# Performance work log

Measured on AMD Instinct MI355X. Metric: run time of the kernel, lower is better.

## Reference

```python
import jax, jax.numpy as jnp
import numpy as np

EMBED_DIM = 1024
NUM_HEADS = 16
HEAD_DIM = EMBED_DIM // NUM_HEADS


def setup_inputs() -> dict:
    key = jax.random.key(0)
    ks = jax.random.split(key, 9)
    B, T, D = 4, 2048, EMBED_DIM
    s = 1.0 / np.sqrt(D)
    inp = {
        "x": jax.random.normal(ks[0], (B, T, D), dtype=jnp.float32),
        "Wq": jax.random.normal(ks[1], (D, D), dtype=jnp.float32) * s,
        "bq": jnp.zeros((D,), dtype=jnp.float32),
        "Wk": jax.random.normal(ks[2], (D, D), dtype=jnp.float32) * s,
        "bk": jnp.zeros((D,), dtype=jnp.float32),
        "Wv": jax.random.normal(ks[3], (D, D), dtype=jnp.float32) * s,
        "bv": jnp.zeros((D,), dtype=jnp.float32),
        "Wo": jax.random.normal(ks[4], (D, D), dtype=jnp.float32) * s,
        "bo": jnp.zeros((D,), dtype=jnp.float32),
    }
    return inp


def _attn(x, Wq, bq, Wk, bk, Wv, bv, Wo, bo):
    B, T, D = x.shape
    H, Hd = NUM_HEADS, HEAD_DIM
    # projections: Linear uses y = x @ W^T + b; here W stored as (D, D) acting as W^T already
    q = (x @ Wq + bq).reshape(B, T, H, Hd).transpose(0, 2, 1, 3)  # [B,H,T,Hd]
    k = (x @ Wk + bk).reshape(B, T, H, Hd).transpose(0, 2, 1, 3)
    v = (x @ Wv + bv).reshape(B, T, H, Hd).transpose(0, 2, 1, 3)
    scores = jnp.einsum("bhqd,bhkd->bhqk", q, k) / np.sqrt(Hd)  # [B,H,T,T]
    causal = jnp.tril(jnp.ones((T, T), dtype=bool))
    scores = jnp.where(causal, scores, -jnp.inf)
    w = jax.nn.softmax(scores, axis=-1)
    out = jnp.einsum("bhqk,bhkd->bhqd", w, v)  # [B,H,T,Hd]
    out = out.transpose(0, 2, 1, 3).reshape(B, T, D)
    return out @ Wo + bo


def reference(x, Wq, bq, Wk, bk, Wv, bv, Wo, bo):
    return _attn(x, Wq, bq, Wk, bk, Wv, bv, Wo, bo)
```

## Files before the change

kernel.cpp:

```cpp
#include <hip/hip_runtime.h>
#include <cstdint>
#include <cstddef>

#define DI __device__ __forceinline__

typedef unsigned short u16;
typedef short bf16x8 __attribute__((ext_vector_type(8)));
typedef unsigned short u16x8 __attribute__((ext_vector_type(8)));
typedef float f32x4 __attribute__((ext_vector_type(4)));

static constexpr int DMODEL = 1024, T = 2048, BB = 4, NH = 16, HD = 64;
static constexpr int M = BB * T;

static constexpr size_t XB_OFF = 0;
static constexpr size_t WT_OFF = (size_t)M * DMODEL;
static constexpr size_t Q_OFF  = WT_OFF + 4ull * DMODEL * DMODEL;
static constexpr size_t K_OFF  = Q_OFF + (size_t)M * DMODEL;
static constexpr size_t V_OFF  = K_OFF + (size_t)M * DMODEL;
static constexpr size_t O_OFF  = XB_OFF;

DI u16 f2bf(float x) {
  unsigned int u = __builtin_bit_cast(unsigned int, x);
  u += 0x7fffu + ((u >> 16) & 1u);
  return (u16)(u >> 16);
}

DI unsigned int cvtpk_bf16(float a, float b) {
  unsigned int r;
  asm("v_cvt_pk_bf16_f32 %0, %1, %2" : "=v"(r) : "v"(a), "v"(b));
  return r;
}

DI void gld_lds16(const void* g, void* l) {
  __builtin_amdgcn_global_load_lds(
      (const __attribute__((address_space(1))) void*)g,
      (__attribute__((address_space(3))) void*)l, 16, 0, 0);
}

__global__ void k_cast(const float* __restrict__ in, u16* __restrict__ out) {
  size_t i = (size_t)(blockIdx.x * 256 + threadIdx.x) * 8;
  float4 a = *(const float4*)(in + i);
  float4 b = *(const float4*)(in + i + 4);
  u16x8 v;
  v[0] = f2bf(a.x); v[1] = f2bf(a.y); v[2] = f2bf(a.z); v[3] = f2bf(a.w);
  v[4] = f2bf(b.x); v[5] = f2bf(b.y); v[6] = f2bf(b.z); v[7] = f2bf(b.w);
  *(u16x8*)(out + i) = v;
}

__global__ void k_transw(const float* __restrict__ Wq, const float* __restrict__ Wk,
                         const float* __restrict__ Wv, const float* __restrict__ Wo,
                         u16* __restrict__ WtBase) {
  __shared__ u16 tile[32][33];
  const int z = blockIdx.z;
  const float* W = z == 0 ? Wq : (z == 1 ? Wk : (z == 2 ? Wv : Wo));
  u16* Wt = WtBase + (size_t)z * DMODEL * DMODEL;
  int tx = threadIdx.x, ty = threadIdx.y;
  int c = blockIdx.x * 32 + tx;
#pragma unroll
  for (int i = 0; i < 4; ++i) {
    int r = blockIdx.y * 32 + ty + i * 8;
    tile[ty + i * 8][tx] = f2bf(W[(size_t)r * DMODEL + c]);
  }
  __syncthreads();
#pragma unroll
  for (int i = 0; i < 4; ++i) {
    int rw = blockIdx.x * 32 + ty + i * 8;
    Wt[(size_t)rw * DMODEL + blockIdx.y * 32 + tx] = tile[tx][ty + i * 8];
  }
}

__launch_bounds__(256, 2)
__global__ void k_gemm_qkv(const u16* __restrict__ A, const u16* __restrict__ Wt,
                           const float* __restrict__ bq, const float* __restrict__ bk,
                           const float* __restrict__ bv,
                           u16* __restrict__ Qo, u16* __restrict__ Ko, u16* __restrict__ Vo) {
  __shared__ u16 As[128 * 64];
  __shared__ u16 Bs[128 * 64];
  const int z = blockIdx.z;
  const u16* Bt = Wt + (size_t)z * DMODEL * DMODEL;
  const float* bias = z == 0 ? bq : (z == 1 ? bk : bv);
  u16* out = z == 0 ? Qo : (z == 1 ? Ko : Vo);
  const float scale = z == 0 ? 0.125f * 1.4426950408889634f : 1.0f;

  const int tid = threadIdx.x;
  const int wave = tid >> 6, lane = tid & 63;
  const int g = lane >> 4, l15 = lane & 15;
  const int brow = blockIdx.x * 128, bcol = blockIdx.y * 128;
  const int wr = wave >> 1, wc = wave & 1;
  const int srow = tid >> 3, schunk = tid & 7;

  f32x4 acc[4][4] = {};

  for (int k0 = 0; k0 < DMODEL; k0 += 64) {
    __syncthreads();
#pragma unroll
    for (int j = 0; j < 4; ++j) {
      int r = j * 32 + srow;
      int cs = (schunk ^ (r & 7)) * 8;
      gld_lds16(A + (size_t)(brow + r) * DMODEL + k0 + cs, (char*)As + j * 4096 + wave * 1024);
      gld_lds16(Bt + (size_t)(bcol + r) * DMODEL + k0 + cs, (char*)Bs + j * 4096 + wave * 1024);
    }
    __syncthreads();
#pragma unroll
    for (int kh = 0; kh < 2; ++kh) {
      bf16x8 af[4], bfr[4];
#pragma unroll
      for (int m = 0; m < 4; ++m) {
        int r = wr * 64 + m * 16 + l15;
        int ch = (kh * 4 + g) ^ (r & 7);
        af[m] = *(const bf16x8*)((const char*)As + r * 128 + ch * 16);
      }
#pragma unroll
      for (int n = 0; n < 4; ++n) {
        int r = wc * 64 + n * 16 + l15;
        int ch = (kh * 4 + g) ^ (r & 7);
        bfr[n] = *(const bf16x8*)((const char*)Bs + r * 128 + ch * 16);
      }
#pragma unroll
      for (int m = 0; m < 4; ++m)
#pragma unroll
        for (int n = 0; n < 4; ++n)
          acc[m][n] = __builtin_amdgcn_mfma_f32_16x16x32_bf16(af[m], bfr[n], acc[m][n], 0, 0, 0);
    }
  }

#pragma unroll
  for (int m = 0; m < 4; ++m)
#pragma unroll
    for (int n = 0; n < 4; ++n) {
      int col = bcol + wc * 64 + n * 16 + l15;
      float bias_v = bias[col];
      int h = col >> 6, d = col & 63;
#pragma unroll
      for (int r = 0; r < 4; ++r) {
        int row = brow + wr * 64 + m * 16 + g * 4 + r;
        int b = row >> 11, t = row & 2047;
        float v = (acc[m][n][r] + bias_v) * scale;
        out[(((size_t)(b * NH + h) * T + t) << 6) + d] = f2bf(v);
      }
    }
}

__launch_bounds__(256, 2)
__global__ void k_gemm_out(const u16* __restrict__ A, const u16* __restrict__ Bt,
                           const float* __restrict__ bias, float* __restrict__ out) {
  __shared__ u16 As[128 * 64];
  __shared__ u16 Bs[128 * 64];
  const int tid = threadIdx.x;
  const int wave = tid >> 6, lane = tid & 63;
  const int g = lane >> 4, l15 = lane & 15;
  const int brow = blockIdx.x * 128, bcol = blockIdx.y * 128;
  const int wr = wave >> 1, wc = wave & 1;
  const int srow = tid >> 3, schunk = tid & 7;

  f32x4 acc[4][4] = {};

  for (int k0 = 0; k0 < DMODEL; k0 += 64) {
    __syncthreads();
#pragma unroll
    for (int j = 0; j < 4; ++j) {
      int r = j * 32 + srow;
      int cs = (schunk ^ (r & 7)) * 8;
      gld_lds16(A + (size_t)(brow + r) * DMODEL + k0 + cs, (char*)As + j * 4096 + wave * 1024);
      gld_lds16(Bt + (size_t)(bcol + r) * DMODEL + k0 + cs, (char*)Bs + j * 4096 + wave * 1024);
    }
    __syncthreads();
#pragma unroll
    for (int kh = 0; kh < 2; ++kh) {
      bf16x8 af[4], bfr[4];
#pragma unroll
      for (int m = 0; m < 4; ++m) {
        int r = wr * 64 + m * 16 + l15;
        int ch = (kh * 4 + g) ^ (r & 7);
        af[m] = *(const bf16x8*)((const char*)As + r * 128 + ch * 16);
      }
#pragma unroll
      for (int n = 0; n < 4; ++n) {
        int r = wc * 64 + n * 16 + l15;
        int ch = (kh * 4 + g) ^ (r & 7);
        bfr[n] = *(const bf16x8*)((const char*)Bs + r * 128 + ch * 16);
      }
#pragma unroll
      for (int m = 0; m < 4; ++m)
#pragma unroll
        for (int n = 0; n < 4; ++n)
          acc[m][n] = __builtin_amdgcn_mfma_f32_16x16x32_bf16(af[m], bfr[n], acc[m][n], 0, 0, 0);
    }
  }

#pragma unroll
  for (int m = 0; m < 4; ++m)
#pragma unroll
    for (int n = 0; n < 4; ++n) {
      int col = bcol + wc * 64 + n * 16 + l15;
      float bias_v = bias[col];
#pragma unroll
      for (int r = 0; r < 4; ++r) {
        int row = brow + wr * 64 + m * 16 + g * 4 + r;
        out[(size_t)row * DMODEL + col] = acc[m][n][r] + bias_v;
      }
    }
}

__launch_bounds__(256, 4)
__global__ void k_attn(const u16* __restrict__ Qw, const u16* __restrict__ Kw,
                       const u16* __restrict__ Vw, u16* __restrict__ Ow) {
  __shared__ u16 Ksh[64 * 64];
  __shared__ u16 Vt[64 * 64];
  __shared__ u16 Plds[4][16 * 64];

  const int tid = threadIdx.x;
  const int wave = tid >> 6, lane = tid & 63;
  const int g = lane >> 4, l15 = lane & 15;
  const int qp = blockIdx.x;
  const int bh = blockIdx.y;
  const u16* Qb = Qw + (size_t)bh * T * HD;
  const u16* Kb = Kw + (size_t)bh * T * HD;
  const u16* Vb = Vw + (size_t)bh * T * HD;
  const int b = bh >> 4, h = bh & 15;
  const int vp = tid & 31, vcg = tid >> 5;
  const int bcast_base = (lane & 48) + ((lane & 48) >> 2);

#pragma unroll
  for (int half = 0; half < 2; ++half) {
    const int qt = half == 0 ? (31 - qp) : qp;
    const int ntiles = qt + 1;

    bf16x8 qf[2];
    {
      int qrow = qt * 64 + wave * 16 + l15;
#pragma unroll
      for (int kh = 0; kh < 2; ++kh)
        qf[kh] = *(const bf16x8*)(Qb + (size_t)qrow * HD + kh * 32 + g * 8);
    }

    f32x4 oacc[4] = {};
    float mrun = -1e30f, lrun = 0.f;

    for (int kt = 0; kt < ntiles; ++kt) {
      __syncthreads();
#pragma unroll
      for (int j = 0; j < 2; ++j) {
        int r = j * 32 + (tid >> 3);
        const u16* gk = Kb + (size_t)(kt * 64 + r) * HD + ((tid & 7) ^ (r & 7)) * 8;
        gld_lds16(gk, (char*)Ksh + j * 4096 + wave * 1024);
      }
      {
        const u16* gv = Vb + (size_t)(kt * 64 + 2 * vp) * HD + vcg * 8;
        bf16x8 v0 = *(const bf16x8*)gv;
        bf16x8 v1 = *(const bf16x8*)(gv + HD);
#pragma unroll
        for (int j = 0; j < 8; ++j) {
          int c = vcg * 8 + j;
          int byteoff = (c * 128 + 4 * vp) ^ ((c & 7) << 4);
          unsigned int pk = (unsigned int)(u16)v0[j] | ((unsigned int)(u16)v1[j] << 16);
          *(unsigned int*)((char*)Vt + byteoff) = pk;
        }
      }
      __syncthreads();

      f32x4 s[4] = {};
#pragma unroll
      for (int kh = 0; kh < 2; ++kh) {
        bf16x8 kf[4];
#pragma unroll
        for (int n = 0; n < 4; ++n) {
          int r = n * 16 + l15;
          int ch = (kh * 4 + g) ^ (r & 7);
          kf[n] = *(const bf16x8*)((const char*)Ksh + r * 128 + ch * 16);
        }
#pragma unroll
        for (int n = 0; n < 4; ++n)
          s[n] = __builtin_amdgcn_mfma_f32_16x16x32_bf16(kf[n], qf[kh], s[n], 0, 0, 0);
      }

      if (kt == qt) {
        int q_in = wave * 16 + l15;
#pragma unroll
        for (int n = 0; n < 4; ++n)
#pragma unroll
          for (int r = 0; r < 4; ++r) {
            int kv_in = n * 16 + g * 4 + r;
            if (kv_in > (half == 0 ? q_in : q_in) || (kv_in > q_in)) {}
            if (kv_in > q_in) s[n][r] = -1e30f;
          }
      }


      float vmax = s[0][0];
#pragma unroll
      for (int n = 0; n < 4; ++n)
#pragma unroll
        for (int r = 0; r < 4; ++r) vmax = fmaxf(vmax, s[n][r]);
      vmax = fmaxf(vmax, __shfl_xor(vmax, 16));
      vmax = fmaxf(vmax, __shfl_xor(vmax, 32));
      float mnew = fmaxf(mrun, vmax);
      float a = exp2f(mrun - mnew);
      mrun = mnew;
      float ps = 0.f;
#pragma unroll
      for (int n = 0; n < 4; ++n)
#pragma unroll
        for (int r = 0; r < 4; ++r) {
          float p = exp2f(s[n][r] - mnew);
          s[n][r] = p;
          ps += p;
        }
      ps += __shfl_xor(ps, 16);
      ps += __shfl_xor(ps, 32);
      lrun = lrun * a + ps;

      float alpha4[4];
#pragma unroll
      for (int r = 0; r < 4; ++r) alpha4[r] = __shfl(a, bcast_base + r);
#pragma unroll
      for (int n = 0; n < 4; ++n)
#pragma unroll
        for (int r = 0; r < 4; ++r) oacc[n][r] *= alpha4[r];

      {
        char* pb = (char*)(Plds[wave]);
#pragma unroll
        for (int n = 0; n < 4; ++n)
#pragma unroll
          for (int i = 0; i < 2; ++i) {
            unsigned int w = cvtpk_bf16(s[n][2 * i], s[n][2 * i + 1]);
            int p = n * 8 + g * 2 + i;
            int off = l15 * 128 + (((p >> 2) ^ (l15 & 7)) << 4) + (p & 3) * 4;
            *(unsigned int*)(pb + off) = w;
          }
      }

#pragma unroll
      for (int kvh = 0; kvh < 2; ++kvh) {
        bf16x8 pa, vb2[4];
        {
          int r = l15;
          int ch = (kvh * 4 + g) ^ (r & 7);
          pa = *(const bf16x8*)((const char*)(Plds[wave]) + r * 128 + ch * 16);
        }
#pragma unroll
        for (int n = 0; n < 4; ++n) {
          int r = n * 16 + l15;
          int ch = (kvh * 4 + g) ^ (r & 7);
          vb2[n] = *(const bf16x8*)((const char*)Vt + r * 128 + ch * 16);
        }
#pragma unroll
        for (int n = 0; n < 4; ++n)
          oacc[n] = __builtin_amdgcn_mfma_f32_16x16x32_bf16(pa, vb2[n], oacc[n], 0, 0, 0);
      }
    }

    float inv = 1.f / lrun;
    float inv4[4];
#pragma unroll
    for (int r = 0; r < 4; ++r) inv4[r] = __shfl(inv, bcast_base + r);
#pragma unroll
    for (int n = 0; n < 4; ++n)
#pragma unroll
      for (int r = 0; r < 4; ++r) {
        int t = qt * 64 + wave * 16 + g * 4 + r;
        int col = h * 64 + n * 16 + l15;
        Ow[((size_t)b * T + t) * DMODEL + col] = f2bf(oacc[n][r] * inv4[r]);
      }
  }
}

extern "C" void kernel_launch(void* const* d_in, const int* in_sizes, int n_in,
                              void* d_out, int out_size, void* d_ws, size_t ws_size,
                              hipStream_t stream) {
  const float* x  = (const float*)d_in[0];
  const float* Wq = (const float*)d_in[1];
  const float* bq = (const float*)d_in[2];
  const float* Wk = (const float*)d_in[3];
  const float* bk = (const float*)d_in[4];
  const float* Wv = (const float*)d_in[5];
  const float* bv = (const float*)d_in[6];
  const float* Wo = (const float*)d_in[7];
  const float* bo = (const float*)d_in[8];
  float* out = (float*)d_out;
  u16* ws = (u16*)d_ws;

  k_cast<<<4096, 256, 0, stream>>>(x, ws + XB_OFF);
  k_transw<<<dim3(32, 32, 4), dim3(32, 8), 0, stream>>>(Wq, Wk, Wv, Wo, ws + WT_OFF);
  k_gemm_qkv<<<dim3(64, 8, 3), 256, 0, stream>>>(ws + XB_OFF, ws + WT_OFF, bq, bk, bv,
                                                 ws + Q_OFF, ws + K_OFF, ws + V_OFF);
  k_attn<<<dim3(16, 64), 256, 0, stream>>>(ws + Q_OFF, ws + K_OFF, ws + V_OFF, ws + O_OFF);
  k_gemm_out<<<dim3(64, 8), 256, 0, stream>>>(ws + O_OFF, ws + WT_OFF + 3ull * DMODEL * DMODEL,
                                              bo, out);
}
```

Measured before the change: 182.9 us.

## Keep P in registers via permlane swap, load K directly, double-buffer V

The attention inner loop now loads K fragments straight from global memory into registers using a permuted row order, instead of staging them through LDS. The P matrix is handed to the PV MFMA through v_permlane32_swap instead of an LDS round trip, which also removes the per-row alpha broadcast shuffles. V is double-buffered in LDS with the next tile prefetched during compute, dropping one barrier per iteration. Output is staged through LDS for coalesced 16-byte stores. The risks are higher register pressure, uncoalesced K loads now issued by every wave, and correctness that depends on the permuted layout matching.

After: 255.6 us. 39.8% more time.

```diff
diff --git a/kernel.cpp b/kernel.cpp
--- a/kernel.cpp
+++ b/kernel.cpp
@@ -205,13 +205,13 @@
 __launch_bounds__(256, 4)
 __global__ void k_attn(const u16* __restrict__ Qw, const u16* __restrict__ Kw,
                        const u16* __restrict__ Vw, u16* __restrict__ Ow) {
-  __shared__ u16 Ksh[64 * 64];
-  __shared__ u16 Vt[64 * 64];
-  __shared__ u16 Plds[4][16 * 64];
+  __shared__ u16 Vt[2][64 * 64];
+  __shared__ u16 Ot[64 * 64];
 
   const int tid = threadIdx.x;
   const int wave = tid >> 6, lane = tid & 63;
   const int g = lane >> 4, l15 = lane & 15;
+  const int tl = (l15 & 3) | ((l15 & 4) << 1) | ((l15 & 8) >> 1);
   const int qp = blockIdx.x;
   const int bh = blockIdx.y;
   const u16* Qb = Qw + (size_t)bh * T * HD;
@@ -219,9 +219,7 @@
   const u16* Vb = Vw + (size_t)bh * T * HD;
   const int b = bh >> 4, h = bh & 15;
   const int vp = tid & 31, vcg = tid >> 5;
-  const int bcast_base = (lane & 48) + ((lane & 48) >> 2);
-
-#pragma unroll
+
   for (int half = 0; half < 2; ++half) {
     const int qt = half == 0 ? (31 - qp) : qp;
     const int ntiles = qt + 1;
@@ -237,42 +235,48 @@
     f32x4 oacc[4] = {};
     float mrun = -1e30f, lrun = 0.f;
 
+    {
+      const u16* gv = Vb + (size_t)(2 * vp) * HD + vcg * 8;
+      bf16x8 v0 = *(const bf16x8*)gv;
+      bf16x8 v1 = *(const bf16x8*)(gv + HD);
+      char* vtb = (char*)(Vt[0]);
+#pragma unroll
+      for (int j = 0; j < 8; ++j) {
+        int c = vcg * 8 + j;
+        int byteoff = (c * 128 + 4 * vp) ^ ((c & 7) << 4);
+        unsigned int pk = (unsigned int)(u16)v0[j] | ((unsigned int)(u16)v1[j] << 16);
+        *(unsigned int*)(vtb + byteoff) = pk;
+      }
+    }
+
     for (int kt = 0; kt < ntiles; ++kt) {
       __syncthreads();
-#pragma unroll
-      for (int j = 0; j < 2; ++j) {
-        int r = j * 32 + (tid >> 3);
-        const u16* gk = Kb + (size_t)(kt * 64 + r) * HD + ((tid & 7) ^ (r & 7)) * 8;
-        gld_lds16(gk, (char*)Ksh + j * 4096 + wave * 1024);
-      }
+      const int cur = kt & 1;
+
+      bf16x8 kf[2][4];
       {
-        const u16* gv = Vb + (size_t)(kt * 64 + 2 * vp) * HD + vcg * 8;
-        bf16x8 v0 = *(const bf16x8*)gv;
-        bf16x8 v1 = *(const bf16x8*)(gv + HD);
-#pragma unroll
-        for (int j = 0; j < 8; ++j) {
-          int c = vcg * 8 + j;
-          int byteoff = (c * 128 + 4 * vp) ^ ((c & 7) << 4);
-          unsigned int pk = (unsigned int)(u16)v0[j] | ((unsigned int)(u16)v1[j] << 16);
-          *(unsigned int*)((char*)Vt + byteoff) = pk;
-        }
-      }
-      __syncthreads();
+        const u16* Kt = Kb + ((size_t)kt << 12);
+#pragma unroll
+        for (int kh = 0; kh < 2; ++kh)
+#pragma unroll
+          for (int n = 0; n < 4; ++n)
+            kf[kh][n] = *(const bf16x8*)(Kt + (size_t)(n * 16 + tl) * HD + kh * 32 + g * 8);
+      }
+
+      bf16x8 v0, v1;
+      const bool havenext = (kt + 1 < ntiles);
+      if (havenext) {
+        const u16* gv = Vb + (size_t)((kt + 1) * 64 + 2 * vp) * HD + vcg * 8;
+        v0 = *(const bf16x8*)gv;
+        v1 = *(const bf16x8*)(gv + HD);
+      }
 
       f32x4 s[4] = {};
 #pragma unroll
-      for (int kh = 0; kh < 2; ++kh) {
-        bf16x8 kf[4];
-#pragma unroll
-        for (int n = 0; n < 4; ++n) {
-          int r = n * 16 + l15;
-          int ch = (kh * 4 + g) ^ (r & 7);
-          kf[n] = *(const bf16x8*)((const char*)Ksh + r * 128 + ch * 16);
-        }
+      for (int kh = 0; kh < 2; ++kh)
 #pragma unroll
         for (int n = 0; n < 4; ++n)
-          s[n] = __builtin_amdgcn_mfma_f32_16x16x32_bf16(kf[n], qf[kh], s[n], 0, 0, 0);
-      }
+          s[n] = __builtin_amdgcn_mfma_f32_16x16x32_bf16(kf[kh][n], qf[kh], s[n], 0, 0, 0);
 
       if (kt == qt) {
         int q_in = wave * 16 + l15;
@@ -280,12 +284,10 @@
         for (int n = 0; n < 4; ++n)
 #pragma unroll
           for (int r = 0; r < 4; ++r) {
-            int kv_in = n * 16 + g * 4 + r;
-            if (kv_in > (half == 0 ? q_in : q_in) || (kv_in > q_in)) {}
+            int kv_in = n * 16 + (g & 1) * 8 + (g >> 1) * 4 + r;
             if (kv_in > q_in) s[n][r] = -1e30f;
           }
       }
-
 
       float vmax = s[0][0];
 #pragma unroll
@@ -309,60 +311,64 @@
       ps += __shfl_xor(ps, 16);
       ps += __shfl_xor(ps, 32);
       lrun = lrun * a + ps;
-
-      float alpha4[4];
-#pragma unroll
-      for (int r = 0; r < 4; ++r) alpha4[r] = __shfl(a, bcast_base + r);
 #pragma unroll
       for (int n = 0; n < 4; ++n)
 #pragma unroll
-        for (int r = 0; r < 4; ++r) oacc[n][r] *= alpha4[r];
-
-      {
-        char* pb = (char*)(Plds[wave]);
-#pragma unroll
-        for (int n = 0; n < 4; ++n)
-#pragma unroll
-          for (int i = 0; i < 2; ++i) {
-            unsigned int w = cvtpk_bf16(s[n][2 * i], s[n][2 * i + 1]);
-            int p = n * 8 + g * 2 + i;
-            int off = l15 * 128 + (((p >> 2) ^ (l15 & 7)) << 4) + (p & 3) * 4;
-            *(unsigned int*)(pb + off) = w;
-          }
-      }
+        for (int r = 0; r < 4; ++r) oacc[n][r] *= a;
 
 #pragma unroll
       for (int kvh = 0; kvh < 2; ++kvh) {
-        bf16x8 pa, vb2[4];
-        {
-          int r = l15;
-          int ch = (kvh * 4 + g) ^ (r & 7);
-          pa = *(const bf16x8*)((const char*)(Plds[wave]) + r * 128 + ch * 16);
+        const int nlo = kvh * 2, nhi = kvh * 2 + 1;
+        unsigned int L0 = cvtpk_bf16(s[nlo][0], s[nlo][1]);
+        unsigned int L1 = cvtpk_bf16(s[nlo][2], s[nlo][3]);
+        unsigned int H0 = cvtpk_bf16(s[nhi][0], s[nhi][1]);
+        unsigned int H1 = cvtpk_bf16(s[nhi][2], s[nhi][3]);
+        asm volatile("v_permlane32_swap_b32 %0, %1" : "+v"(L0), "+v"(H0));
+        asm volatile("v_permlane32_swap_b32 %0, %1" : "+v"(L1), "+v"(H1));
+        bf16x8 pb;
+        unsigned int* pw = (unsigned int*)&pb;
+        pw[0] = L0; pw[1] = L1; pw[2] = H0; pw[3] = H1;
+
+        const int ch = ((kvh * 4 + g) ^ (l15 & 7)) * 16;
+#pragma unroll
+        for (int n = 0; n < 4; ++n) {
+          bf16x8 an = *(const bf16x8*)((const char*)(Vt[cur]) + (n * 16 + l15) * 128 + ch);
+          oacc[n] = __builtin_amdgcn_mfma_f32_16x16x32_bf16(an, pb, oacc[n], 0, 0, 0);
         }
-#pragma unroll
-        for (int n = 0; n < 4; ++n) {
-          int r = n * 16 + l15;
-          int ch = (kvh * 4 + g) ^ (r & 7);
-          vb2[n] = *(const bf16x8*)((const char*)Vt + r * 128 + ch * 16);
+      }
+
+      if (havenext) {
+        char* vtb = (char*)(Vt[cur ^ 1]);
+#pragma unroll
+        for (int j = 0; j < 8; ++j) {
+          int c = vcg * 8 + j;
+          int byteoff = (c * 128 + 4 * vp) ^ ((c & 7) << 4);
+          unsigned int pk = (unsigned int)(u16)v0[j] | ((unsigned int)(u16)v1[j] << 16);
+          *(unsigned int*)(vtb + byteoff) = pk;
         }
-#pragma unroll
-        for (int n = 0; n < 4; ++n)
-          oacc[n] = __builtin_amdgcn_mfma_f32_16x16x32_bf16(pa, vb2[n], oacc[n], 0, 0, 0);
-      }
-    }
-
-    float inv = 1.f / lrun;
-    float inv4[4];
-#pragma unroll
-    for (int r = 0; r < 4; ++r) inv4[r] = __shfl(inv, bcast_base + r);
-#pragma unroll
-    for (int n = 0; n < 4; ++n)
-#pragma unroll
-      for (int r = 0; r < 4; ++r) {
-        int t = qt * 64 + wave * 16 + g * 4 + r;
-        int col = h * 64 + n * 16 + l15;
-        Ow[((size_t)b * T + t) * DMODEL + col] = f2bf(oacc[n][r] * inv4[r]);
-      }
+      }
+    }
+
+    {
+      float inv = 1.f / lrun;
+      char* otb = (char*)Ot;
+#pragma unroll
+      for (int n = 0; n < 4; ++n)
+#pragma unroll
+        for (int i = 0; i < 2; ++i) {
+          unsigned int w = cvtpk_bf16(oacc[n][2 * i] * inv, oacc[n][2 * i + 1] * inv);
+          int didx = n * 8 + g * 2 + i;
+          int off = (wave * 16 + l15) * 128 + ((didx * 4) ^ ((l15 & 7) << 4));
+          *(unsigned int*)(otb + off) = w;
+        }
+      __syncthreads();
+      int q = tid >> 2, seg = tid & 3;
+      uint4 c0 = *(const uint4*)(otb + q * 128 + (((seg * 2) ^ (q & 7)) << 4));
+      uint4 c1 = *(const uint4*)(otb + q * 128 + (((seg * 2 + 1) ^ (q & 7)) << 4));
+      u16* dst = Ow + ((size_t)b * T + qt * 64 + q) * DMODEL + h * 64 + seg * 16;
+      *(uint4*)dst = c0;
+      *(uint4*)(dst + 8) = c1;
+    }
   }
 }
 
```
